# Kernel optimization log

Measured on AMD Instinct MI355X. Metric: run time of the kernel, lower is better.

The kernel has to match this reference:

```python
import jax, jax.numpy as jnp
import numpy as np

N_NODES = 50000
N_EDGES = 800000
IN_DIM = 96
HID_DIM = 96


def setup_inputs() -> dict:
    key = jax.random.key(0)
    ks = jax.random.split(key, 8)
    inputs = jax.random.normal(ks[0], (N_NODES, IN_DIM), dtype=jnp.float32)
    factor = jax.random.uniform(ks[1], (N_EDGES, 1), dtype=jnp.float32)
    src = jax.random.randint(ks[2], (N_EDGES,), 0, N_NODES, dtype=jnp.int32)
    dst = jax.random.randint(ks[3], (N_EDGES,), 0, N_NODES, dtype=jnp.int32)
    # Linear params (torch nn.Linear: y = x @ W.T + b), uniform(-1/sqrt(fan_in), ..)
    s1 = 1.0 / np.sqrt(IN_DIM)
    s2 = 1.0 / np.sqrt(HID_DIM)
    W1 = jax.random.uniform(ks[4], (HID_DIM, IN_DIM), minval=-s1, maxval=s1, dtype=jnp.float32)
    b1 = jax.random.uniform(ks[5], (HID_DIM,), minval=-s1, maxval=s1, dtype=jnp.float32)
    W2 = jax.random.uniform(ks[6], (IN_DIM, HID_DIM), minval=-s2, maxval=s2, dtype=jnp.float32)
    b2 = jax.random.uniform(ks[7], (IN_DIM,), minval=-s2, maxval=s2, dtype=jnp.float32)
    return {"inputs": inputs, "W1": W1, "b1": b1, "W2": W2, "b2": b2,
            "factor": factor, "src": src, "dst": dst}


def _propagate(feat, factor, src, dst, n_nodes):
    # message = h[src] * edge_factor ; reduce = sum at dst
    msg = feat[src] * factor                       # [E, D]
    return jax.ops.segment_sum(msg, dst, num_segments=n_nodes)


def reference(inputs, W1, b1, W2, b2, factor, src, dst):
    n = inputs.shape[0]
    # in-degree norm: deg^{-1/2}, clamped at 1
    deg = jax.ops.segment_sum(jnp.ones((src.shape[0],), inputs.dtype), dst,
                              num_segments=n)
    norm = jnp.maximum(deg, 1.0) ** -0.5           # [N]
    norm = norm[:, None]                           # [N, 1]

    feat = (inputs @ W1.T + b1) * norm             # [N, H]
    h = jnp.tanh(_propagate(feat, factor, src, dst, n))

    feat = (h @ W2.T + b2) * norm                  # [N, D]
    h = jnp.tanh(_propagate(feat, factor, src, dst, n))

    # dgl.mean_nodes over a single graph -> [1, D]; unsqueeze(-1) -> [1, D, 1]
    pooled = jnp.mean(h, axis=0, keepdims=True)[..., None]
    return jnp.tanh(pooled)
```

## Files before the change

kernel.cpp:

```cpp
#include <hip/hip_runtime.h>
#include <math.h>
#include <type_traits>

#define N_NODES 50000
#define N_EDGES 800000
#define DIM 96
#define BCH 12
#define SCAN_BLK 256
#define NBLK ((N_NODES + SCAN_BLK - 1) / SCAN_BLK)
#define GBLK 512
#define NPB 42
#define NBG ((N_NODES + NPB - 1) / NPB)
#define CAP 768
#define R1_ROWS 24
#define R1_BLOCKS ((NBG + R1_ROWS - 1) / R1_ROWS)
#define SC_PASSES 4
#define SC_WIN ((N_NODES + SC_PASSES - 1) / SC_PASSES)
#define F8_SCALE 16.0f
#define F8_INV   0.0625f

typedef short v8s __attribute__((ext_vector_type(8)));
typedef float v4f __attribute__((ext_vector_type(4)));
typedef float v2f __attribute__((ext_vector_type(2)));

__device__ __forceinline__ unsigned short f2bf(float f) {
    unsigned int u = __float_as_uint(f);
    u += 0x7FFFu + ((u >> 16) & 1u);
    return (unsigned short)(u >> 16);
}
__device__ __forceinline__ unsigned int pack2bf(float lo, float hi) {
    return (unsigned int)f2bf(lo) | ((unsigned int)f2bf(hi) << 16);
}

__device__ __forceinline__ float fast_tanh(float x) {
    float ax = fabsf(x);
    float t = __expf(-2.0f * ax);
    float r = (1.0f - t) / (1.0f + t);
    return copysignf(r, x);
}

__device__ __forceinline__ void accf8(float* a, uint2 v, float f) {
    v2f p0 = __builtin_amdgcn_cvt_pk_f32_fp8(v.x, false);
    v2f p1 = __builtin_amdgcn_cvt_pk_f32_fp8(v.x, true);
    v2f p2 = __builtin_amdgcn_cvt_pk_f32_fp8(v.y, false);
    v2f p3 = __builtin_amdgcn_cvt_pk_f32_fp8(v.y, true);
    a[0] += p0.x * f; a[1] += p0.y * f;
    a[2] += p1.x * f; a[3] += p1.y * f;
    a[4] += p2.x * f; a[5] += p2.y * f;
    a[6] += p3.x * f; a[7] += p3.y * f;
}

union U4S8 { uint4 u; v8s s; };


__global__ void count_deg(const int* __restrict__ dst, int* __restrict__ deg,
                          int* __restrict__ rank) {
    int e = blockIdx.x * blockDim.x + threadIdx.x;
    if (e < N_EDGES) rank[e] = atomicAdd(&deg[dst[e]], 1);
}

__global__ void deg_partials(const int* __restrict__ deg, float* __restrict__ norm,
                             int* __restrict__ partials) {
    int b = blockIdx.x, t = threadIdx.x;
    int n = b * SCAN_BLK + t;
    int v = 0;
    if (n < N_NODES) {
        v = deg[n];
        norm[n] = rsqrtf(fmaxf((float)v, 1.0f));
    }
    int s = v;
#pragma unroll
    for (int off = 32; off > 0; off >>= 1) s += __shfl_down(s, off, 64);
    __shared__ int ws_[4];
    if ((t & 63) == 0) ws_[t >> 6] = s;
    __syncthreads();
    if (t == 0) partials[b] = ws_[0] + ws_[1] + ws_[2] + ws_[3];
}

__global__ void scan_partials(const int* __restrict__ partials, int* __restrict__ pprefix) {
    __shared__ int sm[SCAN_BLK];
    int t = threadIdx.x;
    int v = (t < NBLK) ? partials[t] : 0;
    sm[t] = v;
    __syncthreads();
    for (int off = 1; off < SCAN_BLK; off <<= 1) {
        int u = (t >= off) ? sm[t - off] : 0;
        __syncthreads();
        sm[t] += u;
        __syncthreads();
    }
    if (t < NBLK) pprefix[t] = sm[t] - v;
}

__global__ void make_offsets(const int* __restrict__ deg, const int* __restrict__ pprefix,
                             int* __restrict__ offs) {
    __shared__ int sm[SCAN_BLK];
    int b = blockIdx.x, t = threadIdx.x;
    int idx = b * SCAN_BLK + t;
    int v = (idx < N_NODES) ? deg[idx] : 0;
    sm[t] = v;
    __syncthreads();
    for (int off = 1; off < SCAN_BLK; off <<= 1) {
        int u = (t >= off) ? sm[t - off] : 0;
        __syncthreads();
        sm[t] += u;
        __syncthreads();
    }
    if (idx < N_NODES) offs[idx] = pprefix[b] + sm[t] - v;
    if (b == 0 && t == 0) offs[N_NODES] = N_EDGES;
}

__global__ void scatter_edges(const int* __restrict__ src, const int* __restrict__ dst,
                              const float* __restrict__ factor, const int* __restrict__ rank,
                              const int* __restrict__ offs, int2* __restrict__ entries) {
    int tid0 = blockIdx.x * blockDim.x + threadIdx.x;
    int stride = gridDim.x * blockDim.x;
#pragma unroll 1
    for (int pass = 0; pass < SC_PASSES; ++pass) {
        int lo = pass * SC_WIN;
        int hi = min(lo + SC_WIN, N_NODES);
#pragma unroll 1
        for (int e = tid0; e < N_EDGES; e += stride) {
            int d = dst[e];
            if (d >= lo && d < hi) {
                int pos = offs[d] + rank[e];
                entries[pos] = make_int2(src[e], __float_as_int(factor[e]));
            }
        }
    }
}


__global__ void swizzle_W(const float* __restrict__ W, uint4* __restrict__ bsw) {
    int idx = blockIdx.x * blockDim.x + threadIdx.x;
    if (idx >= 18 * 64) return;
    int t = idx >> 6, lane = idx & 63;
    int kt = t / 6, jt = t % 6;
    int quad = lane >> 4, l16 = lane & 15;
    const float4* wp = (const float4*)(W + (size_t)(jt * 16 + l16) * DIM + kt * 32 + quad * 8);
    float4 w0 = wp[0], w1 = wp[1];
    bsw[idx] = make_uint4(pack2bf(w0.x, w0.y), pack2bf(w0.z, w0.w),
                          pack2bf(w1.x, w1.y), pack2bf(w1.z, w1.w));
}


template <typename T>
__global__ __launch_bounds__(256) void gemm_mfma(const T* __restrict__ X,
                                                 const uint4* __restrict__ bsw,
                                                 const float* __restrict__ bias,
                                                 const float* __restrict__ norm,
                                                 unsigned char* __restrict__ out) {
    int tid = threadIdx.x;
    int wave = tid >> 6, lane = tid & 63;
    int quad = lane >> 4, l16 = lane & 15;
    int n0 = blockIdx.x * 64 + wave * 16;
    int node = n0 + l16;
    int rowc = min(node, N_NODES - 1);

    uint4 bfr[18];
#pragma unroll
    for (int t = 0; t < 18; ++t) bfr[t] = bsw[t * 64 + lane];

    v4f acc[6];
#pragma unroll
    for (int jt = 0; jt < 6; ++jt) acc[jt] = (v4f)(0.0f);

#pragma unroll
    for (int kt = 0; kt < 3; ++kt) {
        U4S8 x;
        if constexpr (std::is_same_v<T, float>) {
            const float4* xp = (const float4*)(X + (size_t)rowc * DIM + kt * 32 + quad * 8);
            float4 x0 = xp[0], x1 = xp[1];
            x.u = make_uint4(pack2bf(x0.x, x0.y), pack2bf(x0.z, x0.w),
                             pack2bf(x1.x, x1.y), pack2bf(x1.z, x1.w));
        } else {
            x.u = *(const uint4*)(X + (size_t)rowc * DIM + kt * 32 + quad * 8);
        }
#pragma unroll
        for (int jt = 0; jt < 6; ++jt) {
            U4S8 w; w.u = bfr[kt * 6 + jt];
            acc[jt] = __builtin_amdgcn_mfma_f32_16x16x32_bf16(w.s, x.s, acc[jt], 0, 0, 0);
        }
    }

    if (node < N_NODES) {
        float nm = norm[node] * F8_SCALE;
#pragma unroll
        for (int jt = 0; jt < 6; ++jt) {
            float4 bj = *(const float4*)(bias + jt * 16 + quad * 4);
            float v0 = (acc[jt][0] + bj.x) * nm;
            float v1 = (acc[jt][1] + bj.y) * nm;
            float v2 = (acc[jt][2] + bj.z) * nm;
            float v3 = (acc[jt][3] + bj.w) * nm;
            unsigned int w = (unsigned int)__builtin_amdgcn_cvt_pk_fp8_f32(v0, v1, 0, false);
            w = (unsigned int)__builtin_amdgcn_cvt_pk_fp8_f32(v2, v3, (int)w, true);
            *(unsigned int*)(out + (size_t)node * DIM + jt * 16 + quad * 4) = w;
        }
    }
}


template <bool POOL>
__global__ __launch_bounds__(GBLK) void gather_agg_f8(
        const unsigned char* __restrict__ feat,
        const int* __restrict__ offs,
        const int2* __restrict__ entries,
        unsigned short* __restrict__ out,
        float* __restrict__ partials) {
    __shared__ int2 ents[CAP];
    __shared__ float pool[DIM];
    __shared__ int sh_base, sh_cnt;
    int tid = threadIdx.x;
    int n0 = blockIdx.x * NPB;
    int n1 = min(n0 + NPB, N_NODES);
    if (POOL && tid < DIM) pool[tid] = 0.f;
    if (tid == 0) { sh_base = offs[n0]; sh_cnt = offs[n1] - sh_base; }
    __syncthreads();
    int base = sh_base, cnt = sh_cnt;

    int nl = tid / BCH;
    int c  = tid - nl * BCH;
    int n  = n0 + nl;
    bool active = (tid < NPB * BCH) && (n < N_NODES);
    int lb = 0, le = 0;
    if (active) { lb = offs[n] - base; le = offs[n + 1] - base; }

    float a0[8], a1[8];
#pragma unroll
    for (int i = 0; i < 8; ++i) { a0[i] = 0.f; a1[i] = 0.f; }

    for (int tb = 0; tb < cnt; tb += CAP) {
        int tcnt = min(cnt - tb, CAP);
        if (tb) __syncthreads();
        for (int i = tid; i < tcnt; i += GBLK) ents[i] = entries[base + tb + i];
        __syncthreads();
        int s = max(lb - tb, 0), e = min(le - tb, tcnt);
        int p = s;
        for (; p + 7 < e; p += 8) {
            int2 q0 = ents[p + 0], q1 = ents[p + 1], q2 = ents[p + 2], q3 = ents[p + 3];
            int2 q4 = ents[p + 4], q5 = ents[p + 5], q6 = ents[p + 6], q7 = ents[p + 7];
            uint2 v0 = *((const uint2*)(feat + (size_t)q0.x * DIM) + c);
            uint2 v1 = *((const uint2*)(feat + (size_t)q1.x * DIM) + c);
            uint2 v2 = *((const uint2*)(feat + (size_t)q2.x * DIM) + c);
            uint2 v3 = *((const uint2*)(feat + (size_t)q3.x * DIM) + c);
            uint2 v4 = *((const uint2*)(feat + (size_t)q4.x * DIM) + c);
            uint2 v5 = *((const uint2*)(feat + (size_t)q5.x * DIM) + c);
            uint2 v6 = *((const uint2*)(feat + (size_t)q6.x * DIM) + c);
            uint2 v7 = *((const uint2*)(feat + (size_t)q7.x * DIM) + c);
            accf8(a0, v0, __int_as_float(q0.y));
            accf8(a1, v1, __int_as_float(q1.y));
            accf8(a0, v2, __int_as_float(q2.y));
            accf8(a1, v3, __int_as_float(q3.y));
            accf8(a0, v4, __int_as_float(q4.y));
            accf8(a1, v5, __int_as_float(q5.y));
            accf8(a0, v6, __int_as_float(q6.y));
            accf8(a1, v7, __int_as_float(q7.y));
        }
        for (; p + 3 < e; p += 4) {
            int2 q0 = ents[p], q1 = ents[p + 1], q2 = ents[p + 2], q3 = ents[p + 3];
            uint2 v0 = *((const uint2*)(feat + (size_t)q0.x * DIM) + c);
            uint2 v1 = *((const uint2*)(feat + (size_t)q1.x * DIM) + c);
            uint2 v2 = *((const uint2*)(feat + (size_t)q2.x * DIM) + c);
            uint2 v3 = *((const uint2*)(feat + (size_t)q3.x * DIM) + c);
            accf8(a0, v0, __int_as_float(q0.y));
            accf8(a1, v1, __int_as_float(q1.y));
            accf8(a0, v2, __int_as_float(q2.y));
            accf8(a1, v3, __int_as_float(q3.y));
        }
        for (; p < e; ++p) {
            int2 q0 = ents[p];
            uint2 v0 = *((const uint2*)(feat + (size_t)q0.x * DIM) + c);
            accf8(a0, v0, __int_as_float(q0.y));
        }
    }

#pragma unroll
    for (int i = 0; i < 8; ++i) a0[i] = fast_tanh((a0[i] + a1[i]) * F8_INV);
    if (!POOL) {
        if (active) {
            uint4 o;
            o.x = pack2bf(a0[0], a0[1]);
            o.y = pack2bf(a0[2], a0[3]);
            o.z = pack2bf(a0[4], a0[5]);
            o.w = pack2bf(a0[6], a0[7]);
            ((uint4*)out)[n * BCH + c] = o;
        }
    } else {
        if (active) {
#pragma unroll
            for (int i = 0; i < 8; ++i) atomicAdd(&pool[c * 8 + i], a0[i]);
        }
        __syncthreads();
        if (tid < DIM) partials[(size_t)blockIdx.x * DIM + tid] = pool[tid];
    }
}


__global__ void reduce_stage1(const float* __restrict__ poolpart, float* __restrict__ stage1) {
    __shared__ float pool[DIM];
    int b = blockIdx.x, t = threadIdx.x;
    if (t < DIM) pool[t] = 0.f;
    __syncthreads();
    const int base = b * R1_ROWS * DIM;
    float loc = 0.f;
    int lastc = -1;
    for (int i = t; i < R1_ROWS * DIM; i += 256) {
        int gi = base + i;
        if (gi < NBG * DIM) {
            int col = i % DIM;
            if (col != lastc) {
                if (lastc >= 0) atomicAdd(&pool[lastc], loc);
                lastc = col; loc = 0.f;
            }
            loc += poolpart[gi];
        }
    }
    if (lastc >= 0) atomicAdd(&pool[lastc], loc);
    __syncthreads();
    if (t < DIM) stage1[b * DIM + t] = pool[t];
}

__global__ void reduce_stage2(const float* __restrict__ stage1, float* __restrict__ out) {
    __shared__ float sm[960];
    int t = threadIdx.x;
    int col = t % DIM, slice = t / DIM;
    float s = 0.f;
    for (int k = slice; k < R1_BLOCKS; k += 10) s += stage1[k * DIM + col];
    sm[t] = s;
    __syncthreads();
    if (t < DIM) {
        float tot = 0.f;
#pragma unroll
        for (int i = 0; i < 10; ++i) tot += sm[i * DIM + t];
        out[t] = tanhf(tot * (1.0f / N_NODES));
    }
}


extern "C" void kernel_launch(void* const* d_in, const int* in_sizes, int n_in,
                              void* d_out, int out_size, void* d_ws, size_t ws_size,
                              hipStream_t stream) {
    const float* inputs = (const float*)d_in[0];
    const float* W1     = (const float*)d_in[1];
    const float* b1     = (const float*)d_in[2];
    const float* W2     = (const float*)d_in[3];
    const float* b2     = (const float*)d_in[4];
    const float* factor = (const float*)d_in[5];
    const int*   src    = (const int*)d_in[6];
    const int*   dst    = (const int*)d_in[7];
    float* out = (float*)d_out;

    char* ws = (char*)d_ws;
    int*            deg      = (int*)(ws + 0);
    int*            rank     = (int*)(ws + 262144);
    int*            offs     = (int*)(ws + 3670016);
    float*          norm     = (float*)(ws + 3932160);
    int*            partials = (int*)(ws + 4194304);
    int*            pprefix  = (int*)(ws + 4196352);
    int2*           entries  = (int2*)(ws + 4456448);
    unsigned char*  bufA     = (unsigned char*)(ws + 11534336);
    unsigned short* bufB     = (unsigned short*)(ws + 16777216);
    float*          poolpart = (float*)(ws + 26738688);
    float*          stage1   = (float*)(ws + 27787264);
    uint4*          bsw1     = (uint4*)(ws + 27836416);
    uint4*          bsw2     = (uint4*)(ws + 27856896);

    swizzle_W<<<5, 256, 0, stream>>>(W1, bsw1);
    swizzle_W<<<5, 256, 0, stream>>>(W2, bsw2);

    hipMemsetAsync(deg, 0, N_NODES * sizeof(int), stream);
    count_deg<<<(N_EDGES + 255) / 256, 256, 0, stream>>>(dst, deg, rank);
    deg_partials<<<NBLK, SCAN_BLK, 0, stream>>>(deg, norm, partials);
    scan_partials<<<1, SCAN_BLK, 0, stream>>>(partials, pprefix);
    make_offsets<<<NBLK, SCAN_BLK, 0, stream>>>(deg, pprefix, offs);
    scatter_edges<<<2048, 256, 0, stream>>>(src, dst, factor, rank, offs, entries);

    const int GEMM_BLOCKS = (N_NODES + 63) / 64;

    gemm_mfma<float><<<GEMM_BLOCKS, 256, 0, stream>>>(inputs, bsw1, b1, norm, bufA);
    gather_agg_f8<false><<<NBG, GBLK, 0, stream>>>(bufA, offs, entries, bufB, nullptr);

    gemm_mfma<unsigned short><<<GEMM_BLOCKS, 256, 0, stream>>>(bufB, bsw2, b2, norm, bufA);
    gather_agg_f8<true><<<NBG, GBLK, 0, stream>>>(bufA, offs, entries, nullptr, poolpart);

    reduce_stage1<<<R1_BLOCKS, 256, 0, stream>>>(poolpart, stage1);
    reduce_stage2<<<1, 960, 0, stream>>>(stage1, out);
}
```

Measured before the change: 231.9 us.

## Widen gather to 16-byte lanes, fold norm into edge weights, merge small kernels

Each gather thread now loads 16 fp8 values (uint4) per edge instead of 8, which halves the threads per node and doubles nodes per block and the shared edge capacity. The per-source norm is moved from the GEMM epilogue into the edge factor during scatter. Entry loads become nontemporal. The single-block partial scan is fused into make_offsets and the two weight swizzles into one launch, removing two kernel launches at the cost of every offset block redundantly scanning the partials. Each thread also holds more accumulator registers and the inner loop is unrolled less, so there is less memory-level parallelism per thread.

Result: no change. 234.5 us (+1.1%).

```diff
diff --git a/kernel.cpp b/kernel.cpp
--- a/kernel.cpp
+++ b/kernel.cpp
@@ -5,13 +5,13 @@
 #define N_NODES 50000
 #define N_EDGES 800000
 #define DIM 96
-#define BCH 12
+#define BCH 6
 #define SCAN_BLK 256
 #define NBLK ((N_NODES + SCAN_BLK - 1) / SCAN_BLK)
 #define GBLK 512
-#define NPB 42
+#define NPB 85
 #define NBG ((N_NODES + NPB - 1) / NPB)
-#define CAP 768
+#define CAP 1536
 #define R1_ROWS 24
 #define R1_BLOCKS ((NBG + R1_ROWS - 1) / R1_ROWS)
 #define SC_PASSES 4
@@ -39,15 +39,23 @@
     return copysignf(r, x);
 }
 
-__device__ __forceinline__ void accf8(float* a, uint2 v, float f) {
+__device__ __forceinline__ void accf16(float* a, uint4 v, float f) {
     v2f p0 = __builtin_amdgcn_cvt_pk_f32_fp8(v.x, false);
     v2f p1 = __builtin_amdgcn_cvt_pk_f32_fp8(v.x, true);
     v2f p2 = __builtin_amdgcn_cvt_pk_f32_fp8(v.y, false);
     v2f p3 = __builtin_amdgcn_cvt_pk_f32_fp8(v.y, true);
-    a[0] += p0.x * f; a[1] += p0.y * f;
-    a[2] += p1.x * f; a[3] += p1.y * f;
-    a[4] += p2.x * f; a[5] += p2.y * f;
-    a[6] += p3.x * f; a[7] += p3.y * f;
+    v2f p4 = __builtin_amdgcn_cvt_pk_f32_fp8(v.z, false);
+    v2f p5 = __builtin_amdgcn_cvt_pk_f32_fp8(v.z, true);
+    v2f p6 = __builtin_amdgcn_cvt_pk_f32_fp8(v.w, false);
+    v2f p7 = __builtin_amdgcn_cvt_pk_f32_fp8(v.w, true);
+    a[0]  += p0.x * f; a[1]  += p0.y * f;
+    a[2]  += p1.x * f; a[3]  += p1.y * f;
+    a[4]  += p2.x * f; a[5]  += p2.y * f;
+    a[6]  += p3.x * f; a[7]  += p3.y * f;
+    a[8]  += p4.x * f; a[9]  += p4.y * f;
+    a[10] += p5.x * f; a[11] += p5.y * f;
+    a[12] += p6.x * f; a[13] += p6.y * f;
+    a[14] += p7.x * f; a[15] += p7.y * f;
 }
 
 union U4S8 { uint4 u; v8s s; };
@@ -77,25 +85,20 @@
     if (t == 0) partials[b] = ws_[0] + ws_[1] + ws_[2] + ws_[3];
 }
 
-__global__ void scan_partials(const int* __restrict__ partials, int* __restrict__ pprefix) {
-    __shared__ int sm[SCAN_BLK];
-    int t = threadIdx.x;
-    int v = (t < NBLK) ? partials[t] : 0;
-    sm[t] = v;
-    __syncthreads();
-    for (int off = 1; off < SCAN_BLK; off <<= 1) {
-        int u = (t >= off) ? sm[t - off] : 0;
-        __syncthreads();
-        sm[t] += u;
-        __syncthreads();
-    }
-    if (t < NBLK) pprefix[t] = sm[t] - v;
-}
-
-__global__ void make_offsets(const int* __restrict__ deg, const int* __restrict__ pprefix,
+__global__ void make_offsets(const int* __restrict__ deg, const int* __restrict__ partials,
                              int* __restrict__ offs) {
     __shared__ int sm[SCAN_BLK];
+    __shared__ int sp[SCAN_BLK];
     int b = blockIdx.x, t = threadIdx.x;
+    sp[t] = (t < NBLK) ? partials[t] : 0;
+    __syncthreads();
+    for (int off = 1; off < SCAN_BLK; off <<= 1) {
+        int u = (t >= off) ? sp[t - off] : 0;
+        __syncthreads();
+        sp[t] += u;
+        __syncthreads();
+    }
+    int ppfx = (b > 0) ? sp[b - 1] : 0;
     int idx = b * SCAN_BLK + t;
     int v = (idx < N_NODES) ? deg[idx] : 0;
     sm[t] = v;
@@ -106,13 +109,14 @@
         sm[t] += u;
         __syncthreads();
     }
-    if (idx < N_NODES) offs[idx] = pprefix[b] + sm[t] - v;
+    if (idx < N_NODES) offs[idx] = ppfx + sm[t] - v;
     if (b == 0 && t == 0) offs[N_NODES] = N_EDGES;
 }
 
 __global__ void scatter_edges(const int* __restrict__ src, const int* __restrict__ dst,
                               const float* __restrict__ factor, const int* __restrict__ rank,
-                              const int* __restrict__ offs, int2* __restrict__ entries) {
+                              const int* __restrict__ offs, const float* __restrict__ norm,
+                              int2* __restrict__ entries) {
     int tid0 = blockIdx.x * blockDim.x + threadIdx.x;
     int stride = gridDim.x * blockDim.x;
 #pragma unroll 1
@@ -123,17 +127,23 @@
         for (int e = tid0; e < N_EDGES; e += stride) {
             int d = dst[e];
             if (d >= lo && d < hi) {
+                int s = src[e];
                 int pos = offs[d] + rank[e];
-                entries[pos] = make_int2(src[e], __float_as_int(factor[e]));
+                float f = factor[e] * norm[s];
+                entries[pos] = make_int2(s, __float_as_int(f));
             }
         }
     }
 }
 
 
-__global__ void swizzle_W(const float* __restrict__ W, uint4* __restrict__ bsw) {
-    int idx = blockIdx.x * blockDim.x + threadIdx.x;
-    if (idx >= 18 * 64) return;
+__global__ void swizzle_W2(const float* __restrict__ W1, const float* __restrict__ W2,
+                           uint4* __restrict__ bsw1, uint4* __restrict__ bsw2) {
+    int gidx = blockIdx.x * blockDim.x + threadIdx.x;
+    if (gidx >= 2 * 1152) return;
+    int w = gidx / 1152, idx = gidx % 1152;
+    const float* W = w ? W2 : W1;
+    uint4* bsw = w ? bsw2 : bsw1;
     int t = idx >> 6, lane = idx & 63;
     int kt = t / 6, jt = t % 6;
     int quad = lane >> 4, l16 = lane & 15;
@@ -148,7 +158,6 @@
 __global__ __launch_bounds__(256) void gemm_mfma(const T* __restrict__ X,
                                                  const uint4* __restrict__ bsw,
                                                  const float* __restrict__ bias,
-                                                 const float* __restrict__ norm,
                                                  unsigned char* __restrict__ out) {
     int tid = threadIdx.x;
     int wave = tid >> 6, lane = tid & 63;
@@ -184,14 +193,13 @@
     }
 
     if (node < N_NODES) {
-        float nm = norm[node] * F8_SCALE;
 #pragma unroll
         for (int jt = 0; jt < 6; ++jt) {
             float4 bj = *(const float4*)(bias + jt * 16 + quad * 4);
-            float v0 = (acc[jt][0] + bj.x) * nm;
-            float v1 = (acc[jt][1] + bj.y) * nm;
-            float v2 = (acc[jt][2] + bj.z) * nm;
-            float v3 = (acc[jt][3] + bj.w) * nm;
+            float v0 = (acc[jt][0] + bj.x) * F8_SCALE;
+            float v1 = (acc[jt][1] + bj.y) * F8_SCALE;
+            float v2 = (acc[jt][2] + bj.z) * F8_SCALE;
+            float v3 = (acc[jt][3] + bj.w) * F8_SCALE;
             unsigned int w = (unsigned int)__builtin_amdgcn_cvt_pk_fp8_f32(v0, v1, 0, false);
             w = (unsigned int)__builtin_amdgcn_cvt_pk_fp8_f32(v2, v3, (int)w, true);
             *(unsigned int*)(out + (size_t)node * DIM + jt * 16 + quad * 4) = w;
@@ -225,70 +233,55 @@
     int lb = 0, le = 0;
     if (active) { lb = offs[n] - base; le = offs[n + 1] - base; }
 
-    float a0[8], a1[8];
-#pragma unroll
-    for (int i = 0; i < 8; ++i) { a0[i] = 0.f; a1[i] = 0.f; }
+    float a[16];
+#pragma unroll
+    for (int i = 0; i < 16; ++i) a[i] = 0.f;
 
     for (int tb = 0; tb < cnt; tb += CAP) {
         int tcnt = min(cnt - tb, CAP);
         if (tb) __syncthreads();
-        for (int i = tid; i < tcnt; i += GBLK) ents[i] = entries[base + tb + i];
+        for (int i = tid; i < tcnt; i += GBLK) {
+            long long raw = __builtin_nontemporal_load((const long long*)(entries + base + tb + i));
+            ents[i] = *(int2*)&raw;
+        }
         __syncthreads();
         int s = max(lb - tb, 0), e = min(le - tb, tcnt);
         int p = s;
-        for (; p + 7 < e; p += 8) {
+        for (; p + 3 < e; p += 4) {
             int2 q0 = ents[p + 0], q1 = ents[p + 1], q2 = ents[p + 2], q3 = ents[p + 3];
-            int2 q4 = ents[p + 4], q5 = ents[p + 5], q6 = ents[p + 6], q7 = ents[p + 7];
-            uint2 v0 = *((const uint2*)(feat + (size_t)q0.x * DIM) + c);
-            uint2 v1 = *((const uint2*)(feat + (size_t)q1.x * DIM) + c);
-            uint2 v2 = *((const uint2*)(feat + (size_t)q2.x * DIM) + c);
-            uint2 v3 = *((const uint2*)(feat + (size_t)q3.x * DIM) + c);
-            uint2 v4 = *((const uint2*)(feat + (size_t)q4.x * DIM) + c);
-            uint2 v5 = *((const uint2*)(feat + (size_t)q5.x * DIM) + c);
-            uint2 v6 = *((const uint2*)(feat + (size_t)q6.x * DIM) + c);
-            uint2 v7 = *((const uint2*)(feat + (size_t)q7.x * DIM) + c);
-            accf8(a0, v0, __int_as_float(q0.y));
-            accf8(a1, v1, __int_as_float(q1.y));
-            accf8(a0, v2, __int_as_float(q2.y));
-            accf8(a1, v3, __int_as_float(q3.y));
-            accf8(a0, v4, __int_as_float(q4.y));
-            accf8(a1, v5, __int_as_float(q5.y));
-            accf8(a0, v6, __int_as_float(q6.y));
-            accf8(a1, v7, __int_as_float(q7.y));
-        }
-        for (; p + 3 < e; p += 4) {
-            int2 q0 = ents[p], q1 = ents[p + 1], q2 = ents[p + 2], q3 = ents[p + 3];
-            uint2 v0 = *((const uint2*)(feat + (size_t)q0.x * DIM) + c);
-            uint2 v1 = *((const uint2*)(feat + (size_t)q1.x * DIM) + c);
-            uint2 v2 = *((const uint2*)(feat + (size_t)q2.x * DIM) + c);
-            uint2 v3 = *((const uint2*)(feat + (size_t)q3.x * DIM) + c);
-            accf8(a0, v0, __int_as_float(q0.y));
-            accf8(a1, v1, __int_as_float(q1.y));
-            accf8(a0, v2, __int_as_float(q2.y));
-            accf8(a1, v3, __int_as_float(q3.y));
+            uint4 v0 = *((const uint4*)(feat + (size_t)q0.x * DIM) + c);
+            uint4 v1 = *((const uint4*)(feat + (size_t)q1.x * DIM) + c);
+            uint4 v2 = *((const uint4*)(feat + (size_t)q2.x * DIM) + c);
+            uint4 v3 = *((const uint4*)(feat + (size_t)q3.x * DIM) + c);
+            accf16(a, v0, __int_as_float(q0.y));
+            accf16(a, v1, __int_as_float(q1.y));
+            accf16(a, v2, __int_as_float(q2.y));
+            accf16(a, v3, __int_as_float(q3.y));
         }
         for (; p < e; ++p) {
             int2 q0 = ents[p];
-            uint2 v0 = *((const uint2*)(feat + (size_t)q0.x * DIM) + c);
-            accf8(a0, v0, __int_as_float(q0.y));
-        }
-    }
-
-#pragma unroll
-    for (int i = 0; i < 8; ++i) a0[i] = fast_tanh((a0[i] + a1[i]) * F8_INV);
+            uint4 v0 = *((const uint4*)(feat + (size_t)q0.x * DIM) + c);
+            accf16(a, v0, __int_as_float(q0.y));
+        }
+    }
+
+#pragma unroll
+    for (int i = 0; i < 16; ++i) a[i] = fast_tanh(a[i] * F8_INV);
     if (!POOL) {
         if (active) {
-            uint4 o;
-            o.x = pack2bf(a0[0], a0[1]);
-            o.y = pack2bf(a0[2], a0[3]);
-            o.z = pack2bf(a0[4], a0[5]);
-            o.w = pack2bf(a0[6], a0[7]);
-            ((uint4*)out)[n * BCH + c] = o;
+            uint4 o0, o1;
+            o0.x = pack2bf(a[0], a[1]);   o0.y = pack2bf(a[2], a[3]);
+            o0.z = pack2bf(a[4], a[5]);   o0.w = pack2bf(a[6], a[7]);
+            o1.x = pack2bf(a[8], a[9]);   o1.y = pack2bf(a[10], a[11]);
+            o1.z = pack2bf(a[12], a[13]); o1.w = pack2bf(a[14], a[15]);
+            uint4* op = (uint4*)out + (size_t)n * 12 + c * 2;
+            op[0] = o0;
+            op[1] = o1;
         }
     } else {
         if (active) {
 #pragma unroll
-            for (int i = 0; i < 8; ++i) atomicAdd(&pool[c * 8 + i], a0[i]);
+            for (int i = 0; i < 16; ++i) atomicAdd(&pool[c * 16 + i], a[i]);
         }
         __syncthreads();
         if (tid < DIM) partials[(size_t)blockIdx.x * DIM + tid] = pool[tid];
@@ -356,7 +349,6 @@
     int*            offs     = (int*)(ws + 3670016);
     float*          norm     = (float*)(ws + 3932160);
     int*            partials = (int*)(ws + 4194304);
-    int*            pprefix  = (int*)(ws + 4196352);
     int2*           entries  = (int2*)(ws + 4456448);
     unsigned char*  bufA     = (unsigned char*)(ws + 11534336);
     unsigned short* bufB     = (unsigned short*)(ws + 16777216);
@@ -365,22 +357,20 @@
     uint4*          bsw1     = (uint4*)(ws + 27836416);
     uint4*          bsw2     = (uint4*)(ws + 27856896);
 
-    swizzle_W<<<5, 256, 0, stream>>>(W1, bsw1);
-    swizzle_W<<<5, 256, 0, stream>>>(W2, bsw2);
+    swizzle_W2<<<9, 256, 0, stream>>>(W1, W2, bsw1, bsw2);
 
     hipMemsetAsync(deg, 0, N_NODES * sizeof(int), stream);
     count_deg<<<(N_EDGES + 255) / 256, 256, 0, stream>>>(dst, deg, rank);
     deg_partials<<<NBLK, SCAN_BLK, 0, stream>>>(deg, norm, partials);
-    scan_partials<<<1, SCAN_BLK, 0, stream>>>(partials, pprefix);
-    make_offsets<<<NBLK, SCAN_BLK, 0, stream>>>(deg, pprefix, offs);
-    scatter_edges<<<2048, 256, 0, stream>>>(src, dst, factor, rank, offs, entries);
+    make_offsets<<<NBLK, SCAN_BLK, 0, stream>>>(deg, partials, offs);
+    scatter_edges<<<2048, 256, 0, stream>>>(src, dst, factor, rank, offs, norm, entries);
 
     const int GEMM_BLOCKS = (N_NODES + 63) / 64;
 
-    gemm_mfma<float><<<GEMM_BLOCKS, 256, 0, stream>>>(inputs, bsw1, b1, norm, bufA);
+    gemm_mfma<float><<<GEMM_BLOCKS, 256, 0, stream>>>(inputs, bsw1, b1, bufA);
     gather_agg_f8<false><<<NBG, GBLK, 0, stream>>>(bufA, offs, entries, bufB, nullptr);
 
-    gemm_mfma<unsigned short><<<GEMM_BLOCKS, 256, 0, stream>>>(bufB, bsw2, b2, norm, bufA);
+    gemm_mfma<unsigned short><<<GEMM_BLOCKS, 256, 0, stream>>>(bufB, bsw2, b2, bufA);
     gather_agg_f8<true><<<NBG, GBLK, 0, stream>>>(bufA, offs, entries, nullptr, poolpart);
 
     reduce_stage1<<<R1_BLOCKS, 256, 0, stream>>>(poolpart, stage1);
```
